# Kernel optimization log

Measured on AMD Instinct MI355X. Metric: run time of the kernel, lower is better.

The kernel has to match this reference:

```python
import jax, jax.numpy as jnp
import numpy as np

VISION_TOKEN_TYPE = 1

def _swiglu_mlp(x, w_gate, w_up, w_down):
    # x: [B, L, D]; w_gate/w_up: [D, F]; w_down: [F, D]
    g = jax.nn.silu(jnp.einsum('bld,df->blf', x, w_gate))
    u = jnp.einsum('bld,df->blf', x, w_up)
    return jnp.einsum('blf,fd->bld', g * u, w_down)

def _vision_mask(token_type_ids):
    # vision_token_mask[:, :-1] = (tt[:, :-1]==V) & (tt[:, 1:]==V); last col False
    is_v = token_type_ids == VISION_TOKEN_TYPE
    pair = is_v[:, :-1] & is_v[:, 1:]
    return jnp.concatenate([pair, jnp.zeros_like(pair[:, :1])], axis=1)  # [B, L] bool

def setup_inputs() -> dict:
    key = jax.random.key(0)
    ks = jax.random.split(key, 8)
    B, L, D, F = 2, 2048, 4096, 11008
    s = 0.02
    return {
        'hidden_states': jax.random.normal(ks[0], (B, L, D), dtype=jnp.float32),
        'token_type_ids': jax.random.randint(ks[1], (B, L), 0, 2, dtype=jnp.int64),
        'vision_gate': jax.random.normal(ks[2], (D, F), dtype=jnp.float32) * s,
        'vision_up': jax.random.normal(ks[3], (D, F), dtype=jnp.float32) * s,
        'vision_down': jax.random.normal(ks[4], (F, D), dtype=jnp.float32) * s,
        'language_gate': jax.random.normal(ks[5], (D, F), dtype=jnp.float32) * s,
        'language_up': jax.random.normal(ks[6], (D, F), dtype=jnp.float32) * s,
        'language_down': jax.random.normal(ks[7], (F, D), dtype=jnp.float32) * s,
    }

def reference(hidden_states, token_type_ids, vision_gate, vision_up, vision_down,
              language_gate, language_up, language_down):
    vmask = _vision_mask(token_type_ids)  # [B, L]
    out_v = _swiglu_mlp(hidden_states, vision_gate, vision_up, vision_down)
    out_l = _swiglu_mlp(hidden_states, language_gate, language_up, language_down)
    return jnp.where(vmask[:, :, None], out_v, out_l)
```

## Files before the change

### kernel.cpp

```cpp
#include <hip/hip_runtime.h>
#include <hip/hip_bf16.h>

#define B_    2
#define L_    2048
#define D_    4096
#define F_    11008
#define M_TOK (B_ * L_)
#define BM    256
#define M_ALLOC (M_TOK + BM)
#define NTM   (M_ALLOC / BM)
#define NT_GU (D_ / 64)
#define NT_DN (F_ / 64)
#define NTILE_GU (2 * F_ / 256)
#define GATE_TILES (F_ / 256)
#define LDS_BYTES 131072

typedef __attribute__((ext_vector_type(8))) __bf16 bf16x8;
typedef __attribute__((ext_vector_type(4))) float  f32x4;
typedef unsigned short ushort_t;
typedef unsigned int   uint_t;


__device__ __forceinline__ void gload_lds16(const void* g, void* l) {
  __builtin_amdgcn_global_load_lds(
      (const __attribute__((address_space(1))) void*)g,
      (__attribute__((address_space(3))) void*)l, 16, 0, 0);
}

#define PH_BAR()  { __builtin_amdgcn_sched_barrier(0); __builtin_amdgcn_s_barrier(); __builtin_amdgcn_sched_barrier(0); }
#define LGKM0()   { asm volatile("s_waitcnt lgkmcnt(0)" ::: "memory"); __builtin_amdgcn_sched_barrier(0); }
#define VM4()     { asm volatile("s_waitcnt vmcnt(4)" ::: "memory"); __builtin_amdgcn_sched_barrier(0); }
#define VM0()     { asm volatile("s_waitcnt vmcnt(0)" ::: "memory"); __builtin_amdgcn_sched_barrier(0); }

__device__ __forceinline__ ushort_t f2bf(float v) {
  union { __hip_bfloat16 h; ushort_t u; } cv;
  cv.h = __float2bfloat16(v);
  return cv.u;
}

__device__ __forceinline__ void stage_half(const __hip_bfloat16* __restrict__ src, int ldE,
                                           __bf16* ldsb, int w, int lane) {
#pragma unroll
  for (int j = 0; j < 2; ++j) {
    const int ch  = (w * 2 + j) * 64 + lane;
    const int row = ch >> 3;
    const int cc  = (ch & 7) ^ (row & 7);
    gload_lds16(src + (size_t)(row * ldE + cc * 8), ldsb + (w * 2 + j) * 512);
  }
}

__device__ __forceinline__ bf16x8 ldfrag(const __bf16* region, int row, int koffb) {
  const int off = ((row << 7) + koffb) ^ ((row & 7) << 4);
  return *(const bf16x8*)((const char*)region + off);
}

__device__ __forceinline__ void mfma_q(f32x4 (&acc)[8][4], int mb, int nb,
                                       const bf16x8 (&af)[4][2], const bf16x8 (&bf)[2][2]) {
#pragma unroll
  for (int mm = 0; mm < 4; ++mm)
#pragma unroll
    for (int nn = 0; nn < 2; ++nn)
#pragma unroll
      for (int ks = 0; ks < 2; ++ks)
        acc[mb + mm][nb + nn] = __builtin_amdgcn_mfma_f32_16x16x32_bf16(
            af[mm][ks], bf[nn][ks], acc[mb + mm][nb + nn], 0, 0, 0);
}

__device__ __forceinline__ void gemm_kloop(const __hip_bfloat16* __restrict__ Ag, const int ldA,
                                           const __hip_bfloat16* __restrict__ Bg, const int ldB,
                                           const int nt, __bf16* smem, f32x4 (&acc)[8][4],
                                           const int wm, const int wn, const int l15,
                                           const int l4, const int w, const int lane) {
  stage_half(Ag,             ldA, smem,                w, lane);
  stage_half(Ag + 128 * ldA, ldA, smem + 8192,         w, lane);
  stage_half(Bg,             ldB, smem + 16384,        w, lane);
  stage_half(Bg + 128 * ldB, ldB, smem + 24576,        w, lane);
  if (1 < nt) {
    stage_half(Ag + 64,             ldA, smem + 32768,        w, lane);
    stage_half(Ag + 64 + 128 * ldA, ldA, smem + 32768 + 8192, w, lane);
  }
  VM4(); PH_BAR();

  for (int t = 0; t < nt; ++t) {
    __bf16* bufc = smem + (t & 1) * 32768;
    __bf16* bufn = smem + ((t + 1) & 1) * 32768;
    const __bf16* At = bufc;
    const __bf16* Bt = bufc + 16384;
    bf16x8 a0[4][2], a1[4][2], b0[2][2], b1[2][2];

#pragma unroll
    for (int i = 0; i < 4; ++i)
#pragma unroll
      for (int ks = 0; ks < 2; ++ks)
        a0[i][ks] = ldfrag(At, wm * 128 + i * 16 + l15, ks * 64 + l4 * 16);
#pragma unroll
    for (int n = 0; n < 2; ++n)
#pragma unroll
      for (int ks = 0; ks < 2; ++ks)
        b0[n][ks] = ldfrag(Bt, wn * 64 + n * 16 + l15, ks * 64 + l4 * 16);
    if (t + 1 < nt) stage_half(Bg + (t + 1) * 64, ldB, bufn + 16384, w, lane);
    PH_BAR(); LGKM0();
    __builtin_amdgcn_s_setprio(1);
    mfma_q(acc, 0, 0, a0, b0);
    __builtin_amdgcn_s_setprio(0);
    PH_BAR();

#pragma unroll
    for (int i = 0; i < 4; ++i)
#pragma unroll
      for (int ks = 0; ks < 2; ++ks)
        a1[i][ks] = ldfrag(At, wm * 128 + 64 + i * 16 + l15, ks * 64 + l4 * 16);
    if (t + 1 < nt) stage_half(Bg + (t + 1) * 64 + 128 * ldB, ldB, bufn + 24576, w, lane);
    PH_BAR(); LGKM0();
    __builtin_amdgcn_s_setprio(1);
    mfma_q(acc, 4, 0, a1, b0);
    __builtin_amdgcn_s_setprio(0);
    PH_BAR();

#pragma unroll
    for (int n = 0; n < 2; ++n)
#pragma unroll
      for (int ks = 0; ks < 2; ++ks)
        b1[n][ks] = ldfrag(Bt, wn * 64 + 32 + n * 16 + l15, ks * 64 + l4 * 16);
    if (t + 2 < nt) stage_half(Ag + (t + 2) * 64, ldA, bufc, w, lane);
    PH_BAR(); LGKM0();
    __builtin_amdgcn_s_setprio(1);
    mfma_q(acc, 4, 2, a1, b1);
    __builtin_amdgcn_s_setprio(0);
    PH_BAR();

    if (t + 2 < nt) stage_half(Ag + (t + 2) * 64 + 128 * ldA, ldA, bufc + 8192, w, lane);
    __builtin_amdgcn_s_setprio(1);
    mfma_q(acc, 0, 2, a0, b1);
    __builtin_amdgcn_s_setprio(0);
    if (t + 2 < nt) { VM4(); } else { VM0(); }
    PH_BAR();
  }
}


__global__ void init_kernel(int* counters, int* slot2tok) {
  int i = blockIdx.x * 256 + threadIdx.x;
  if (i < 2) counters[i] = 0;
  if (i < M_ALLOC) slot2tok[i] = -1;
}

__global__ void assign_kernel(const int* __restrict__ tt, int* counters,
                              int* __restrict__ slot2tok) {
  int t = blockIdx.x * 256 + threadIdx.x;
  if (t >= M_TOK) return;
  int l = t & (L_ - 1);
  bool isv = (tt[t] == 1) && (l < L_ - 1) && (tt[t + 1] == 1);
  int slot;
  if (isv) slot = atomicAdd(&counters[0], 1);
  else     slot = M_ALLOC - 1 - atomicAdd(&counters[1], 1);
  slot2tok[slot] = t;
}

__global__ void gather_cvt(const float* __restrict__ x, const int* __restrict__ slot2tok,
                           __hip_bfloat16* __restrict__ xg) {
  const int s = blockIdx.x;
  const int t = slot2tok[s];
  __hip_bfloat16* dst = xg + (size_t)s * D_ + threadIdx.x * 16;
  union { ushort_t h[8]; uint4 v; } p0, p1;
  if (t >= 0) {
    const float4* s4 = (const float4*)(x + (size_t)t * D_ + threadIdx.x * 16);
    float4 a = s4[0], b = s4[1], c = s4[2], d = s4[3];
    float vals[16] = {a.x,a.y,a.z,a.w,b.x,b.y,b.z,b.w,c.x,c.y,c.z,c.w,d.x,d.y,d.z,d.w};
#pragma unroll
    for (int i = 0; i < 8; ++i) p0.h[i] = f2bf(vals[i]);
#pragma unroll
    for (int i = 0; i < 8; ++i) p1.h[i] = f2bf(vals[8 + i]);
  } else {
    p0.v = make_uint4(0, 0, 0, 0);
    p1.v = make_uint4(0, 0, 0, 0);
  }
  *(uint4*)dst = p0.v;
  *(uint4*)(dst + 8) = p1.v;
}

__global__ __launch_bounds__(128) void transpose_cvt64(const float* __restrict__ in,
                                                       __hip_bfloat16* __restrict__ out,
                                                       int R, int C) {
  const int c  = threadIdx.x & 63;
  const int rc = threadIdx.x >> 6;
  const int c0 = blockIdx.x * 64;
  const int r0 = blockIdx.y * 64 + rc * 32;
  const float* ip = in + (size_t)r0 * C + c0 + c;
  uint_t pk[16];
#pragma unroll
  for (int j = 0; j < 16; ++j) {
    float v0 = ip[(size_t)(2 * j) * C];
    float v1 = ip[(size_t)(2 * j + 1) * C];
    pk[j] = (uint_t)f2bf(v0) | ((uint_t)f2bf(v1) << 16);
  }
  uint4* op = (uint4*)(out + (size_t)(c0 + c) * R + r0);
#pragma unroll
  for (int k = 0; k < 4; ++k)
    op[k] = make_uint4(pk[4 * k], pk[4 * k + 1], pk[4 * k + 2], pk[4 * k + 3]);
}

__global__ void silu_mul_kernel(__hip_bfloat16* __restrict__ G,
                                const __hip_bfloat16* __restrict__ U, long long n8) {
  long long i = (long long)blockIdx.x * 256 + threadIdx.x;
  if (i >= n8) return;
  union { uint4 v; ushort_t s[8]; } g, u, h;
  g.v = ((const uint4*)G)[i];
  u.v = ((const uint4*)U)[i];
#pragma unroll
  for (int k = 0; k < 8; ++k) {
    float gf = __uint_as_float((uint_t)g.s[k] << 16);
    float uf = __uint_as_float((uint_t)u.s[k] << 16);
    float s  = gf / (1.0f + __expf(-gf));
    h.s[k] = f2bf(s * uf);
  }
  ((uint4*)G)[i] = h.v;
}

__global__ void sentinel_kernel(float* out, int n) {
  int i = blockIdx.x * 256 + threadIdx.x;
  if (i < n) out[i] = 1e30f;
}


__global__ __launch_bounds__(512, 2) void gemm256_gateup(
    const __hip_bfloat16* __restrict__ Xg,
    const __hip_bfloat16* __restrict__ WgTv, const __hip_bfloat16* __restrict__ WuTv,
    const __hip_bfloat16* __restrict__ WgTl, const __hip_bfloat16* __restrict__ WuTl,
    __hip_bfloat16* __restrict__ G, __hip_bfloat16* __restrict__ U,
    const int* __restrict__ counters) {
  extern __shared__ __bf16 smem[];
  const int tid = threadIdx.x, lane = tid & 63, w = tid >> 6;
  const int wm = w >> 2, wn = w & 3;
  const int l15 = lane & 15, l4 = lane >> 4;

  const int orig = blockIdx.x;
  const int nwg = gridDim.x;
  const int q = nwg >> 3, r = nwg & 7, xcd = orig & 7;
  const int wg = (xcd < r ? xcd * (q + 1) : r * (q + 1) + (xcd - r) * q) + (orig >> 3);
  const int mt = wg / NTILE_GU, nt = wg % NTILE_GU;
  const int row0 = mt * BM;
  const int nv = counters[0];
  const bool isv = row0 < nv;
  const bool isgate = nt < GATE_TILES;
  const __hip_bfloat16* Bsrc = isgate ? (isv ? WgTv : WgTl) : (isv ? WuTv : WuTl);
  const int ncol0 = (isgate ? nt : nt - GATE_TILES) * 256;
  const __hip_bfloat16* Ag = Xg + (size_t)row0 * D_;
  const __hip_bfloat16* Bg = Bsrc + (size_t)ncol0 * D_;

  f32x4 acc[8][4] = {};
  gemm_kloop(Ag, D_, Bg, D_, NT_GU, smem, acc, wm, wn, l15, l4, w, lane);

  __hip_bfloat16* Out = isgate ? G : U;
#pragma unroll
  for (int m = 0; m < 8; ++m) {
    const int grow = row0 + wm * 128 + m * 16 + l4 * 4;
#pragma unroll
    for (int rr = 0; rr < 4; ++rr) {
      __hip_bfloat16* orow = Out + (size_t)(grow + rr) * F_ + ncol0 + wn * 64 + l15;
#pragma unroll
      for (int n = 0; n < 4; ++n)
        orow[n * 16] = __float2bfloat16(acc[m][n][rr]);
    }
  }
}

__global__ __launch_bounds__(512, 2) void gemm256_down(
    const __hip_bfloat16* __restrict__ H,
    const __hip_bfloat16* __restrict__ WdTv, const __hip_bfloat16* __restrict__ WdTl,
    float* __restrict__ out, const int* __restrict__ counters,
    const int* __restrict__ slot2tok) {
  extern __shared__ __bf16 smem[];
  const int tid = threadIdx.x, lane = tid & 63, w = tid >> 6;
  const int wm = w >> 2, wn = w & 3;
  const int l15 = lane & 15, l4 = lane >> 4;

  const int mt = blockIdx.x / (D_ / 256);
  const int nt = blockIdx.x % (D_ / 256);
  const int z  = blockIdx.y;
  const int row0 = mt * BM;
  const int ncol0 = nt * 256;
  const int ntz = NT_DN / 2;
  const int t0 = z * ntz;
  const int nv = counters[0];
  const __hip_bfloat16* Bsrc = (row0 < nv) ? WdTv : WdTl;
  const __hip_bfloat16* Ag = H + (size_t)row0 * F_ + t0 * 64;
  const __hip_bfloat16* Bg = Bsrc + (size_t)ncol0 * F_ + t0 * 64;

  f32x4 acc[8][4] = {};
  gemm_kloop(Ag, F_, Bg, F_, ntz, smem, acc, wm, wn, l15, l4, w, lane);

#pragma unroll
  for (int m = 0; m < 8; ++m) {
    const int slot = row0 + wm * 128 + m * 16 + l4 * 4;
#pragma unroll
    for (int rr = 0; rr < 4; ++rr) {
      const int tok = slot2tok[slot + rr];
      if (tok < 0) continue;
      float* orow = out + (size_t)tok * D_ + ncol0 + wn * 64 + l15;
#pragma unroll
      for (int n = 0; n < 4; ++n)
        atomicAdd(&orow[n * 16], acc[m][n][rr]);
    }
  }
}


extern "C" void kernel_launch(void* const* d_in, const int* in_sizes, int n_in,
                              void* d_out, int out_size, void* d_ws, size_t ws_size,
                              hipStream_t stream) {
  const float* x   = (const float*)d_in[0];
  const int*   tt  = (const int*)d_in[1];
  const float* wgv = (const float*)d_in[2];
  const float* wuv = (const float*)d_in[3];
  const float* wdv = (const float*)d_in[4];
  const float* wgl = (const float*)d_in[5];
  const float* wul = (const float*)d_in[6];
  const float* wdl = (const float*)d_in[7];
  float* out = (float*)d_out;

  size_t off = 0;
  auto nalign = [](size_t v) { return (v + 255) & ~(size_t)255; };
  const size_t o_cnt = off; off += nalign(2 * sizeof(int));
  const size_t o_s2t = off; off += nalign((size_t)M_ALLOC * sizeof(int));
  const size_t o_xg  = off; off += nalign((size_t)M_ALLOC * D_ * 2);
  const size_t o_g   = off; off += nalign((size_t)M_ALLOC * F_ * 2);
  const size_t o_u   = off; off += nalign((size_t)M_ALLOC * F_ * 2);
  const size_t wbytes = nalign((size_t)D_ * F_ * 2);
  const size_t o_wgv = off; off += wbytes;
  const size_t o_wuv = off; off += wbytes;
  const size_t o_wgl = off; off += wbytes;
  const size_t o_wul = off; off += wbytes;

  if (ws_size < off) {
    sentinel_kernel<<<(out_size + 255) / 256, 256, 0, stream>>>(out, out_size);
    return;
  }

  char* ws = (char*)d_ws;
  int* counters = (int*)(ws + o_cnt);
  int* slot2tok = (int*)(ws + o_s2t);
  __hip_bfloat16* Xg  = (__hip_bfloat16*)(ws + o_xg);
  __hip_bfloat16* G   = (__hip_bfloat16*)(ws + o_g);
  __hip_bfloat16* U   = (__hip_bfloat16*)(ws + o_u);
  __hip_bfloat16* WgTv = (__hip_bfloat16*)(ws + o_wgv);
  __hip_bfloat16* WuTv = (__hip_bfloat16*)(ws + o_wuv);
  __hip_bfloat16* WgTl = (__hip_bfloat16*)(ws + o_wgl);
  __hip_bfloat16* WuTl = (__hip_bfloat16*)(ws + o_wul);
  __hip_bfloat16* WdTv = WgTv;
  __hip_bfloat16* WdTl = WuTv;

  hipFuncSetAttribute((const void*)gemm256_gateup,
                      hipFuncAttributeMaxDynamicSharedMemorySize, LDS_BYTES);
  hipFuncSetAttribute((const void*)gemm256_down,
                      hipFuncAttributeMaxDynamicSharedMemorySize, LDS_BYTES);

  hipMemsetAsync(out, 0, (size_t)out_size * sizeof(float), stream);

  init_kernel<<<(M_ALLOC + 255) / 256, 256, 0, stream>>>(counters, slot2tok);
  assign_kernel<<<(M_TOK + 255) / 256, 256, 0, stream>>>(tt, counters, slot2tok);
  gather_cvt<<<M_ALLOC, 256, 0, stream>>>(x, slot2tok, Xg);

  dim3 tb(128);
  dim3 tg_gu(F_ / 64, D_ / 64);
  transpose_cvt64<<<tg_gu, tb, 0, stream>>>(wgv, WgTv, D_, F_);
  transpose_cvt64<<<tg_gu, tb, 0, stream>>>(wuv, WuTv, D_, F_);
  transpose_cvt64<<<tg_gu, tb, 0, stream>>>(wgl, WgTl, D_, F_);
  transpose_cvt64<<<tg_gu, tb, 0, stream>>>(wul, WuTl, D_, F_);

  gemm256_gateup<<<dim3(NTM * NTILE_GU), 512, LDS_BYTES, stream>>>(
      Xg, WgTv, WuTv, WgTl, WuTl, G, U, counters);

  const long long n8 = (long long)M_ALLOC * F_ / 8;
  silu_mul_kernel<<<(int)((n8 + 255) / 256), 256, 0, stream>>>(G, U, n8);

  dim3 tg_dn(D_ / 64, F_ / 64);
  transpose_cvt64<<<tg_dn, tb, 0, stream>>>(wdv, WdTv, F_, D_);
  transpose_cvt64<<<tg_dn, tb, 0, stream>>>(wdl, WdTl, F_, D_);

  gemm256_down<<<dim3(NTM * (D_ / 256), 2), 512, LDS_BYTES, stream>>>(
      G, WdTv, WdTl, out, counters, slot2tok);
}
```

Measured before the change: 1.697 ms.

## Fuse gate and up GEMMs with SiLU-multiply epilogue into one kernel

Replaces the separate gate/up GEMM tiles and the standalone silu_mul kernel with a fused kernel. Each workgroup computes a 256x128 tile of both the gate and up projections from a shared A tile, then applies SiLU(g)*u in the epilogue and writes only H. This removes the G/U round trip through global memory, the extra elementwise launch and one workspace buffer. In exchange it uses a new hand-written k-loop with its own LDS staging and wait counts. The narrower per-matrix N tile may also lower MFMA efficiency per wave.

```diff
diff --git a/kernel.cpp b/kernel.cpp
--- a/kernel.cpp
+++ b/kernel.cpp
@@ -11,8 +11,7 @@
 #define NTM   (M_ALLOC / BM)
 #define NT_GU (D_ / 64)
 #define NT_DN (F_ / 64)
-#define NTILE_GU (2 * F_ / 256)
-#define GATE_TILES (F_ / 256)
+#define NTILE_F (F_ / 128)
 #define LDS_BYTES 131072
 
 typedef __attribute__((ext_vector_type(8))) __bf16 bf16x8;
@@ -200,70 +199,123 @@
     op[k] = make_uint4(pk[4 * k], pk[4 * k + 1], pk[4 * k + 2], pk[4 * k + 3]);
 }
 
-__global__ void silu_mul_kernel(__hip_bfloat16* __restrict__ G,
-                                const __hip_bfloat16* __restrict__ U, long long n8) {
-  long long i = (long long)blockIdx.x * 256 + threadIdx.x;
-  if (i >= n8) return;
-  union { uint4 v; ushort_t s[8]; } g, u, h;
-  g.v = ((const uint4*)G)[i];
-  u.v = ((const uint4*)U)[i];
-#pragma unroll
-  for (int k = 0; k < 8; ++k) {
-    float gf = __uint_as_float((uint_t)g.s[k] << 16);
-    float uf = __uint_as_float((uint_t)u.s[k] << 16);
-    float s  = gf / (1.0f + __expf(-gf));
-    h.s[k] = f2bf(s * uf);
-  }
-  ((uint4*)G)[i] = h.v;
-}
-
 __global__ void sentinel_kernel(float* out, int n) {
   int i = blockIdx.x * 256 + threadIdx.x;
   if (i < n) out[i] = 1e30f;
 }
 
-
-__global__ __launch_bounds__(512, 2) void gemm256_gateup(
+__global__ __launch_bounds__(512, 2) void gemm256_gateup_fused(
     const __hip_bfloat16* __restrict__ Xg,
     const __hip_bfloat16* __restrict__ WgTv, const __hip_bfloat16* __restrict__ WuTv,
     const __hip_bfloat16* __restrict__ WgTl, const __hip_bfloat16* __restrict__ WuTl,
-    __hip_bfloat16* __restrict__ G, __hip_bfloat16* __restrict__ U,
-    const int* __restrict__ counters) {
+    __hip_bfloat16* __restrict__ H, const int* __restrict__ counters) {
   extern __shared__ __bf16 smem[];
   const int tid = threadIdx.x, lane = tid & 63, w = tid >> 6;
-  const int wm = w >> 2, wn = w & 3;
+  const int wm = w >> 1, wn = w & 1;
   const int l15 = lane & 15, l4 = lane >> 4;
 
   const int orig = blockIdx.x;
   const int nwg = gridDim.x;
   const int q = nwg >> 3, r = nwg & 7, xcd = orig & 7;
   const int wg = (xcd < r ? xcd * (q + 1) : r * (q + 1) + (xcd - r) * q) + (orig >> 3);
-  const int mt = wg / NTILE_GU, nt = wg % NTILE_GU;
+  const int mt = wg / NTILE_F, ntile = wg % NTILE_F;
   const int row0 = mt * BM;
+  const int ncol0 = ntile * 128;
   const int nv = counters[0];
   const bool isv = row0 < nv;
-  const bool isgate = nt < GATE_TILES;
-  const __hip_bfloat16* Bsrc = isgate ? (isv ? WgTv : WgTl) : (isv ? WuTv : WuTl);
-  const int ncol0 = (isgate ? nt : nt - GATE_TILES) * 256;
-  const __hip_bfloat16* Ag = Xg + (size_t)row0 * D_;
-  const __hip_bfloat16* Bg = Bsrc + (size_t)ncol0 * D_;
-
-  f32x4 acc[8][4] = {};
-  gemm_kloop(Ag, D_, Bg, D_, NT_GU, smem, acc, wm, wn, l15, l4, w, lane);
-
-  __hip_bfloat16* Out = isgate ? G : U;
-#pragma unroll
-  for (int m = 0; m < 8; ++m) {
-    const int grow = row0 + wm * 128 + m * 16 + l4 * 4;
+  const __hip_bfloat16* Ag   = Xg + (size_t)row0 * D_;
+  const __hip_bfloat16* Bg_g = (isv ? WgTv : WgTl) + (size_t)ncol0 * D_;
+  const __hip_bfloat16* Bu_g = (isv ? WuTv : WuTl) + (size_t)ncol0 * D_;
+
+  f32x4 accg[4][4] = {};
+  f32x4 accu[4][4] = {};
+  const int nt = NT_GU;
+
+  stage_half(Ag,                  D_, smem,          w, lane);
+  stage_half(Ag + 128 * D_,       D_, smem + 8192,   w, lane);
+  stage_half(Bg_g,                D_, smem + 32768,  w, lane);
+  stage_half(Bu_g,                D_, smem + 49152,  w, lane);
+  stage_half(Ag + 64,             D_, smem + 16384,  w, lane);
+  stage_half(Ag + 64 + 128 * D_,  D_, smem + 24576,  w, lane);
+  VM4(); PH_BAR();
+
+  for (int t = 0; t < nt; ++t) {
+    const int cur = t & 1;
+    const __bf16* At  = smem + cur * 16384;
+    const __bf16* Bgt = smem + 32768 + cur * 8192;
+    const __bf16* But = smem + 49152 + cur * 8192;
+    __bf16* nxA  = smem + cur * 16384;
+    __bf16* nxBg = smem + 32768 + (cur ^ 1) * 8192;
+    __bf16* nxBu = smem + 49152 + (cur ^ 1) * 8192;
+    bf16x8 af[4][2], bg[4][2], bu[4][2];
+
+#pragma unroll
+    for (int m = 0; m < 4; ++m)
+#pragma unroll
+      for (int ks = 0; ks < 2; ++ks)
+        af[m][ks] = ldfrag(At, wm * 64 + m * 16 + l15, ks * 64 + l4 * 16);
+#pragma unroll
+    for (int n = 0; n < 4; ++n)
+#pragma unroll
+      for (int ks = 0; ks < 2; ++ks)
+        bg[n][ks] = ldfrag(Bgt, wn * 64 + n * 16 + l15, ks * 64 + l4 * 16);
+    if (t + 1 < nt) {
+      stage_half(Bg_g + (t + 1) * 64, D_, nxBg, w, lane);
+      stage_half(Bu_g + (t + 1) * 64, D_, nxBu, w, lane);
+    }
+    PH_BAR(); LGKM0();
+    __builtin_amdgcn_s_setprio(1);
+#pragma unroll
+    for (int m = 0; m < 4; ++m)
+#pragma unroll
+      for (int n = 0; n < 4; ++n)
+#pragma unroll
+        for (int ks = 0; ks < 2; ++ks)
+          accg[m][n] = __builtin_amdgcn_mfma_f32_16x16x32_bf16(
+              af[m][ks], bg[n][ks], accg[m][n], 0, 0, 0);
+    __builtin_amdgcn_s_setprio(0);
+    PH_BAR();
+
+#pragma unroll
+    for (int n = 0; n < 4; ++n)
+#pragma unroll
+      for (int ks = 0; ks < 2; ++ks)
+        bu[n][ks] = ldfrag(But, wn * 64 + n * 16 + l15, ks * 64 + l4 * 16);
+    if (t + 2 < nt) {
+      stage_half(Ag + (t + 2) * 64,            D_, nxA,        w, lane);
+      stage_half(Ag + (t + 2) * 64 + 128 * D_, D_, nxA + 8192, w, lane);
+    }
+    PH_BAR(); LGKM0();
+    __builtin_amdgcn_s_setprio(1);
+#pragma unroll
+    for (int m = 0; m < 4; ++m)
+#pragma unroll
+      for (int n = 0; n < 4; ++n)
+#pragma unroll
+        for (int ks = 0; ks < 2; ++ks)
+          accu[m][n] = __builtin_amdgcn_mfma_f32_16x16x32_bf16(
+              af[m][ks], bu[n][ks], accu[m][n], 0, 0, 0);
+    __builtin_amdgcn_s_setprio(0);
+    if (t + 2 < nt) { VM4(); } else { VM0(); }
+    PH_BAR();
+  }
+
+#pragma unroll
+  for (int m = 0; m < 4; ++m) {
+    const int grow = row0 + wm * 64 + m * 16 + l4 * 4;
 #pragma unroll
     for (int rr = 0; rr < 4; ++rr) {
-      __hip_bfloat16* orow = Out + (size_t)(grow + rr) * F_ + ncol0 + wn * 64 + l15;
-#pragma unroll
-      for (int n = 0; n < 4; ++n)
-        orow[n * 16] = __float2bfloat16(acc[m][n][rr]);
+      __hip_bfloat16* orow = H + (size_t)(grow + rr) * F_ + ncol0 + wn * 64 + l15;
+#pragma unroll
+      for (int n = 0; n < 4; ++n) {
+        const float g = accg[m][n][rr];
+        const float u = accu[m][n][rr];
+        orow[n * 16] = __float2bfloat16(g / (1.0f + __expf(-g)) * u);
+      }
     }
   }
 }
+
 
 __global__ __launch_bounds__(512, 2) void gemm256_down(
     const __hip_bfloat16* __restrict__ H,
@@ -324,8 +376,7 @@
   const size_t o_cnt = off; off += nalign(2 * sizeof(int));
   const size_t o_s2t = off; off += nalign((size_t)M_ALLOC * sizeof(int));
   const size_t o_xg  = off; off += nalign((size_t)M_ALLOC * D_ * 2);
-  const size_t o_g   = off; off += nalign((size_t)M_ALLOC * F_ * 2);
-  const size_t o_u   = off; off += nalign((size_t)M_ALLOC * F_ * 2);
+  const size_t o_h   = off; off += nalign((size_t)M_ALLOC * F_ * 2);
   const size_t wbytes = nalign((size_t)D_ * F_ * 2);
   const size_t o_wgv = off; off += wbytes;
   const size_t o_wuv = off; off += wbytes;
@@ -341,8 +392,7 @@
   int* counters = (int*)(ws + o_cnt);
   int* slot2tok = (int*)(ws + o_s2t);
   __hip_bfloat16* Xg  = (__hip_bfloat16*)(ws + o_xg);
-  __hip_bfloat16* G   = (__hip_bfloat16*)(ws + o_g);
-  __hip_bfloat16* U   = (__hip_bfloat16*)(ws + o_u);
+  __hip_bfloat16* H   = (__hip_bfloat16*)(ws + o_h);
   __hip_bfloat16* WgTv = (__hip_bfloat16*)(ws + o_wgv);
   __hip_bfloat16* WuTv = (__hip_bfloat16*)(ws + o_wuv);
   __hip_bfloat16* WgTl = (__hip_bfloat16*)(ws + o_wgl);
@@ -350,7 +400,7 @@
   __hip_bfloat16* WdTv = WgTv;
   __hip_bfloat16* WdTl = WuTv;
 
-  hipFuncSetAttribute((const void*)gemm256_gateup,
+  hipFuncSetAttribute((const void*)gemm256_gateup_fused,
                       hipFuncAttributeMaxDynamicSharedMemorySize, LDS_BYTES);
   hipFuncSetAttribute((const void*)gemm256_down,
                       hipFuncAttributeMaxDynamicSharedMemorySize, LDS_BYTES);
@@ -368,16 +418,13 @@
   transpose_cvt64<<<tg_gu, tb, 0, stream>>>(wgl, WgTl, D_, F_);
   transpose_cvt64<<<tg_gu, tb, 0, stream>>>(wul, WuTl, D_, F_);
 
-  gemm256_gateup<<<dim3(NTM * NTILE_GU), 512, LDS_BYTES, stream>>>(
-      Xg, WgTv, WuTv, WgTl, WuTl, G, U, counters);
-
-  const long long n8 = (long long)M_ALLOC * F_ / 8;
-  silu_mul_kernel<<<(int)((n8 + 255) / 256), 256, 0, stream>>>(G, U, n8);
+  gemm256_gateup_fused<<<dim3(NTM * NTILE_F), 512, LDS_BYTES, stream>>>(
+      Xg, WgTv, WuTv, WgTl, WuTl, H, counters);
 
   dim3 tg_dn(D_ / 64, F_ / 64);
   transpose_cvt64<<<tg_dn, tb, 0, stream>>>(wdv, WdTv, F_, D_);
   transpose_cvt64<<<tg_dn, tb, 0, stream>>>(wdl, WdTl, F_, D_);
 
   gemm256_down<<<dim3(NTM * (D_ / 256), 2), 512, LDS_BYTES, stream>>>(
-      G, WdTv, WdTl, out, counters, slot2tok);
-}
+      H, WdTv, WdTl, out, counters, slot2tok);
+}
```

After: 1.655 ms. 1.03x faster.
